# Kernel optimization log

Measured on AMD Instinct MI355X. Metric: run time of the kernel, lower is better.

The kernel has to match this reference:

```python
import jax, jax.numpy as jnp
import numpy as np

ALPHA = 32.0
LN_EPS = 1e-5

def _cdist(a, b):
    # a: [C, M, K], b: [C, N, K] -> [C, M, N] euclidean distances
    d2 = (jnp.sum(a * a, -1)[:, :, None]
          + jnp.sum(b * b, -1)[:, None, :]
          - 2.0 * jnp.einsum('cmk,cnk->cmn', a, b))
    return jnp.sqrt(jnp.maximum(d2, 1e-12))

def setup_inputs() -> dict:
    key = jax.random.key(0)
    k1, k2 = jax.random.split(key)
    B, D, H, W, C = 8, 16, 28, 28, 256
    CN, SS = 128, 28 * 28
    x = jax.random.normal(k1, (B, D, H, W, C), dtype=jnp.float32)
    ln_weight = jnp.ones((C,), dtype=jnp.float32)
    ln_bias = jnp.zeros((C,), dtype=jnp.float32)
    cluster_center = jax.random.uniform(k2, (C, CN, SS), dtype=jnp.float32)
    return {"x": x, "ln_weight": ln_weight, "ln_bias": ln_bias,
            "cluster_center": cluster_center}

def reference(x, ln_weight, ln_bias, cluster_center):
    B, D, H, W, C = x.shape
    CN = cluster_center.shape[1]
    # LayerNorm over last dim (feature_dim)
    mu = jnp.mean(x, -1, keepdims=True)
    var = jnp.mean(jnp.square(x - mu), -1, keepdims=True)
    xn = (x - mu) * jax.lax.rsqrt(var + LN_EPS) * ln_weight + ln_bias
    # B D H W C -> C (B D) (H W)
    x_re = jnp.transpose(xn, (4, 0, 1, 2, 3)).reshape(C, B * D, H * W)
    soft_assign = _cdist(x_re, cluster_center)          # [C, B*D, CN]
    # C (B D) CN -> B D C CN
    x_distance = jnp.transpose(soft_assign.reshape(C, B, D, CN), (1, 2, 0, 3))
    # NegSoftAssign: exp(-alpha*(x - min)) normalized == softmax(-alpha*x)
    x_distance_assign = jax.nn.softmax(-ALPHA * x_distance, axis=-1)
    cluster_dist = _cdist(cluster_center, cluster_center)  # [C, CN, CN]
    return (x_distance, x_distance_assign, cluster_dist)
```

## Files before the change

kernel.cpp:

```cpp
#include <hip/hip_runtime.h>
#include <hip/hip_bf16.h>
#include <math.h>

#define C_DIM 256
#define BD    128
#define HW    784
#define CN    128
#define KPAD  800

typedef short bf16x8 __attribute__((ext_vector_type(8)));
typedef float f32x4 __attribute__((ext_vector_type(4)));

__device__ inline ushort f2b(float f) {
  unsigned u = __float_as_uint(f);
  unsigned r = (u + 0x7FFFu + ((u >> 16) & 1u)) >> 16;
  return (ushort)r;
}

__global__ __launch_bounds__(256) void ln_transpose_kernel(
    const float* __restrict__ x, const float* __restrict__ lnw,
    const float* __restrict__ lnb, ushort* __restrict__ xre,
    float* __restrict__ anorm) {
  __shared__ ushort btile[256 * 66];
  __shared__ float nbuf[4][256];
  const int t = threadIdx.x, bd = blockIdx.y, bx = blockIdx.x;
  const int hw0 = bx * 64;
  const int w = t >> 6, lane = t & 63;
  const int q = lane >> 4, l = lane & 15;
  const bool last = (bx == 12);
  const int ngroups = last ? 1 : 4;
  const int rpw = ngroups * 4;
  float4 wv[4], bv[4];
  for (int s = 0; s < 4; ++s) {
    wv[s] = *(const float4*)(lnw + s * 64 + l * 4);
    bv[s] = *(const float4*)(lnb + s * 64 + l * 4);
  }
  float nrm[4][4];
  for (int s = 0; s < 4; ++s)
    for (int j = 0; j < 4; ++j) nrm[s][j] = 0.f;
  const float* xb = x + ((size_t)bd * HW + hw0) * 256 + l * 4;
  for (int g = 0; g < ngroups; ++g) {
    int r = w * rpw + g * 4 + q;
    float4 v[4];
    for (int s = 0; s < 4; ++s)
      v[s] = *(const float4*)(xb + (size_t)r * 256 + s * 64);
    float sum = 0.f;
    for (int s = 0; s < 4; ++s) sum += v[s].x + v[s].y + v[s].z + v[s].w;
    for (int off = 1; off <= 8; off <<= 1) sum += __shfl_xor(sum, off, 64);
    float mu = sum * (1.f / 256.f);
    float var = 0.f;
    for (int s = 0; s < 4; ++s) {
      float dx = v[s].x - mu, dy = v[s].y - mu, dz = v[s].z - mu, dw2 = v[s].w - mu;
      var += dx * dx + dy * dy + dz * dz + dw2 * dw2;
    }
    for (int off = 1; off <= 8; off <<= 1) var += __shfl_xor(var, off, 64);
    float sc = rsqrtf(var * (1.f / 256.f) + 1e-5f);
    for (int s = 0; s < 4; ++s) {
      float y0 = (v[s].x - mu) * sc * wv[s].x + bv[s].x;
      float y1 = (v[s].y - mu) * sc * wv[s].y + bv[s].y;
      float y2 = (v[s].z - mu) * sc * wv[s].z + bv[s].z;
      float y3 = (v[s].w - mu) * sc * wv[s].w + bv[s].w;
      nrm[s][0] = fmaf(y0, y0, nrm[s][0]);
      nrm[s][1] = fmaf(y1, y1, nrm[s][1]);
      nrm[s][2] = fmaf(y2, y2, nrm[s][2]);
      nrm[s][3] = fmaf(y3, y3, nrm[s][3]);
      int c = s * 64 + l * 4;
      btile[(c + 0) * 66 + r] = f2b(y0);
      btile[(c + 1) * 66 + r] = f2b(y1);
      btile[(c + 2) * 66 + r] = f2b(y2);
      btile[(c + 3) * 66 + r] = f2b(y3);
    }
  }
  for (int s = 0; s < 4; ++s)
    for (int j = 0; j < 4; ++j) {
      float v = nrm[s][j];
      v += __shfl_xor(v, 16, 64);
      v += __shfl_xor(v, 32, 64);
      nrm[s][j] = v;
    }
  if (q == 0)
    for (int s = 0; s < 4; ++s)
      for (int j = 0; j < 4; ++j) nbuf[w][s * 64 + l * 4 + j] = nrm[s][j];
  __syncthreads();
  float tot = nbuf[0][t] + nbuf[1][t] + nbuf[2][t] + nbuf[3][t];
  atomicAdd(&anorm[t * 128 + bd], tot);
  if (!last) {
    for (int i = 0; i < 32; ++i) {
      int c = w * 64 + i * 2 + (lane >> 5);
      int hwp = (lane & 31) * 2;
      uint val = *(const uint*)&btile[c * 66 + hwp];
      *(uint*)(xre + (size_t)c * (BD * KPAD) + (size_t)bd * KPAD + hw0 + hwp) = val;
    }
  } else {
    for (int i = 0; i < 8; ++i) {
      int c = w * 64 + i * 8 + (lane >> 3);
      int hwp = (lane & 7) * 2;
      uint val = *(const uint*)&btile[c * 66 + hwp];
      ushort* gp = xre + (size_t)c * (BD * KPAD) + (size_t)bd * KPAD + 768;
      *(uint*)(gp + hwp) = val;
      *(uint*)(gp + 16 + hwp) = 0u;
    }
  }
}

__global__ __launch_bounds__(256) void cc_convert_kernel(
    const float* __restrict__ cc, ushort* __restrict__ ccb,
    float* __restrict__ bnorm) {
  int b = blockIdx.x, c = b >> 2;
  int t = threadIdx.x, w = t >> 6, lane = t & 63;
  int r0 = (b & 3) * 32 + w * 8;
  for (int it = 0; it < 8; ++it) {
    int r = r0 + it;
    const float4* src = (const float4*)(cc + ((size_t)c * CN + r) * HW);
    ushort* dst = ccb + (size_t)c * (CN * KPAD) + (size_t)r * KPAD;
    float nrm = 0.f;
    for (int f = lane; f < 196; f += 64) {
      float4 v = src[f];
      nrm = fmaf(v.x, v.x, nrm); nrm = fmaf(v.y, v.y, nrm);
      nrm = fmaf(v.z, v.z, nrm); nrm = fmaf(v.w, v.w, nrm);
      ushort4 o; o.x = f2b(v.x); o.y = f2b(v.y); o.z = f2b(v.z); o.w = f2b(v.w);
      *(ushort4*)(dst + f * 4) = o;
    }
    for (int off = 32; off >= 1; off >>= 1) nrm += __shfl_xor(nrm, off, 64);
    if (lane == 0) bnorm[c * 128 + r] = nrm;
    if (lane < 4) *(ushort4*)(dst + 784 + lane * 4) = make_ushort4(0, 0, 0, 0);
  }
}

__global__ __launch_bounds__(256, 2) void gemm_mfma_kernel(
    const ushort* __restrict__ xre, const ushort* __restrict__ ccb,
    const float* __restrict__ anorm, const float* __restrict__ bnorm,
    float* __restrict__ out_d, float* __restrict__ out_s,
    float* __restrict__ out_c) {
  __shared__ __align__(16) ushort At[512 * 8];
  __shared__ __align__(16) ushort Bt[512 * 8];
  __shared__ float smin[2][128];
  __shared__ float ssum[2][128];
  const int c = blockIdx.x, mode = blockIdx.y;
  const int t = threadIdx.x, w = t >> 6, lane = t & 63;
  const int quad = lane >> 4, ln = lane & 15;
  const int wrow = (w >> 1) * 64, wcol = (w & 1) * 64;
  const ushort* Ag = (mode ? ccb : xre) + (size_t)c * (128 * KPAD);
  const ushort* Bg = ccb + (size_t)c * (128 * KPAD);

  f32x4 acc[4][4];
  for (int i = 0; i < 4; ++i)
    for (int j = 0; j < 4; ++j) acc[i][j] = f32x4{0.f, 0.f, 0.f, 0.f};

  const int ci0 = 128 * w;
  const int row0 = (ci0 + lane) >> 2;
  const int row1 = (ci0 + 64 + lane) >> 2;
  const int q0 = (lane & 3) ^ (row0 & 3);
  const int q1 = (lane & 3) ^ (row1 & 3);
  const ushort* ga0 = Ag + (size_t)row0 * KPAD + q0 * 8;
  const ushort* ga1 = Ag + (size_t)row1 * KPAD + q1 * 8;
  const ushort* gb0 = Bg + (size_t)row0 * KPAD + q0 * 8;
  const ushort* gb1 = Bg + (size_t)row1 * KPAD + q1 * 8;
  ushort* la0 = &At[ci0 * 8];
  ushort* la1 = &At[(ci0 + 64) * 8];
  ushort* lb0 = &Bt[ci0 * 8];
  ushort* lb1 = &Bt[(ci0 + 64) * 8];

  for (int k0 = 0; k0 < 25; ++k0) {
    __syncthreads();
    int kb = k0 * 32;
    __builtin_amdgcn_global_load_lds(
        (const __attribute__((address_space(1))) unsigned int*)(ga0 + kb),
        (__attribute__((address_space(3))) unsigned int*)la0, 16, 0, 0);
    __builtin_amdgcn_global_load_lds(
        (const __attribute__((address_space(1))) unsigned int*)(ga1 + kb),
        (__attribute__((address_space(3))) unsigned int*)la1, 16, 0, 0);
    __builtin_amdgcn_global_load_lds(
        (const __attribute__((address_space(1))) unsigned int*)(gb0 + kb),
        (__attribute__((address_space(3))) unsigned int*)lb0, 16, 0, 0);
    __builtin_amdgcn_global_load_lds(
        (const __attribute__((address_space(1))) unsigned int*)(gb1 + kb),
        (__attribute__((address_space(3))) unsigned int*)lb1, 16, 0, 0);
    __syncthreads();
    bf16x8 af[4], bf[4];
    for (int i = 0; i < 4; ++i) {
      int m = wrow + i * 16 + ln;
      af[i] = *(const bf16x8*)&At[(m * 4 + (quad ^ (m & 3))) * 8];
    }
    for (int j = 0; j < 4; ++j) {
      int n = wcol + j * 16 + ln;
      bf[j] = *(const bf16x8*)&Bt[(n * 4 + (quad ^ (n & 3))) * 8];
    }
    for (int i = 0; i < 4; ++i)
      for (int j = 0; j < 4; ++j)
        acc[i][j] = __builtin_amdgcn_mfma_f32_16x16x32_bf16(af[i], bf[j], acc[i][j], 0, 0, 0);
  }

  const float* rn = (mode ? bnorm : anorm) + c * 128;
  const float* cn = bnorm + c * 128;
  float cnv[4];
  for (int j = 0; j < 4; ++j) cnv[j] = cn[wcol + j * 16 + ln];
  float d[4][4][4];
  for (int i = 0; i < 4; ++i) {
    float rv[4];
    for (int r = 0; r < 4; ++r) rv[r] = rn[wrow + i * 16 + quad * 4 + r];
    for (int j = 0; j < 4; ++j)
      for (int r = 0; r < 4; ++r) {
        float d2 = rv[r] + cnv[j] - 2.f * acc[i][j][r];
        d[i][j][r] = sqrtf(fmaxf(d2, 1e-12f));
      }
  }

  if (mode) {
    float* ob = out_c + (size_t)c * (128 * 128);
    for (int i = 0; i < 4; ++i)
      for (int r = 0; r < 4; ++r) {
        int m = wrow + i * 16 + quad * 4 + r;
        for (int j = 0; j < 4; ++j) ob[m * 128 + wcol + j * 16 + ln] = d[i][j][r];
      }
  } else {
    int half = w & 1;
    for (int i = 0; i < 4; ++i)
      for (int r = 0; r < 4; ++r) {
        int m = wrow + i * 16 + quad * 4 + r;
        size_t ob = ((size_t)m * 256 + c) * 128 + wcol;
        for (int j = 0; j < 4; ++j) out_d[ob + j * 16 + ln] = d[i][j][r];
        float mn = fminf(fminf(d[i][0][r], d[i][1][r]), fminf(d[i][2][r], d[i][3][r]));
        for (int off = 1; off < 16; off <<= 1) mn = fminf(mn, __shfl_xor(mn, off, 64));
        if (ln == 0) smin[half][m] = mn;
      }
    __syncthreads();
    for (int i = 0; i < 4; ++i)
      for (int r = 0; r < 4; ++r) {
        int m = wrow + i * 16 + quad * 4 + r;
        float mn = fminf(smin[0][m], smin[1][m]);
        float s = 0.f;
        for (int j = 0; j < 4; ++j) {
          float e = __expf(-32.f * (d[i][j][r] - mn));
          d[i][j][r] = e;
          s += e;
        }
        for (int off = 1; off < 16; off <<= 1) s += __shfl_xor(s, off, 64);
        if (ln == 0) ssum[half][m] = s;
      }
    __syncthreads();
    for (int i = 0; i < 4; ++i)
      for (int r = 0; r < 4; ++r) {
        int m = wrow + i * 16 + quad * 4 + r;
        float inv = 1.f / (ssum[0][m] + ssum[1][m]);
        size_t ob = ((size_t)m * 256 + c) * 128 + wcol;
        for (int j = 0; j < 4; ++j) out_s[ob + j * 16 + ln] = d[i][j][r] * inv;
      }
  }
}

extern "C" void kernel_launch(void* const* d_in, const int* in_sizes, int n_in,
                              void* d_out, int out_size, void* d_ws, size_t ws_size,
                              hipStream_t stream) {
  const float* x   = (const float*)d_in[0];
  const float* lnw = (const float*)d_in[1];
  const float* lnb = (const float*)d_in[2];
  const float* cc  = (const float*)d_in[3];
  float* out   = (float*)d_out;
  float* out_d = out;
  float* out_s = out + 4194304;
  float* out_c = out + 8388608;

  ushort* xre_b = (ushort*)d_ws;
  ushort* cc_b  = xre_b + 26214400;
  float*  anorm = (float*)(cc_b + 26214400);
  float*  bnorm = anorm + 32768;

  hipMemsetAsync(anorm, 0, 32768 * sizeof(float), stream);
  ln_transpose_kernel<<<dim3(13, 128), 256, 0, stream>>>(x, lnw, lnb, xre_b, anorm);
  cc_convert_kernel<<<1024, 256, 0, stream>>>(cc, cc_b, bnorm);
  gemm_mfma_kernel<<<dim3(256, 2), 256, 0, stream>>>(xre_b, cc_b, anorm, bnorm,
                                                     out_d, out_s, out_c);
}
```

Before: 309.9 us.

## Double-buffer GEMM LDS loads, shrink LN/convert tiles, single-pass LN stats

The GEMM now double-buffers its LDS tiles, prefetching the next K slice while the current one feeds the MFMAs, and drops one barrier per iteration. Mode-1 blocks (cluster vs cluster) skip loading B and reuse the A tile. The grid is flattened so each cluster's two modes are adjacent, which may share the center tile in cache. The LayerNorm/transpose kernel uses 32-wide HW tiles with more blocks and computes variance in one pass as E[x^2]-mu^2, which is slightly less numerically robust. The cc conversion is spread over twice as many blocks, one row per 16 lanes.

```diff
diff --git a/kernel.cpp b/kernel.cpp
--- a/kernel.cpp
+++ b/kernel.cpp
@@ -21,15 +21,18 @@
     const float* __restrict__ x, const float* __restrict__ lnw,
     const float* __restrict__ lnb, ushort* __restrict__ xre,
     float* __restrict__ anorm) {
-  __shared__ ushort btile[256 * 66];
+  __shared__ ushort btile[256 * 36];
   __shared__ float nbuf[4][256];
   const int t = threadIdx.x, bd = blockIdx.y, bx = blockIdx.x;
-  const int hw0 = bx * 64;
+  const int hw0 = bx * 32;
   const int w = t >> 6, lane = t & 63;
   const int q = lane >> 4, l = lane & 15;
-  const bool last = (bx == 12);
-  const int ngroups = last ? 1 : 4;
+  const bool last = (bx == 24);
+  const int ngroups = last ? 1 : 2;
   const int rpw = ngroups * 4;
+  if (last) {
+    for (int r = 16; r < 32; ++r) btile[t * 36 + r] = 0;
+  }
   float4 wv[4], bv[4];
   for (int s = 0; s < 4; ++s) {
     wv[s] = *(const float4*)(lnw + s * 64 + l * 4);
@@ -44,17 +47,19 @@
     float4 v[4];
     for (int s = 0; s < 4; ++s)
       v[s] = *(const float4*)(xb + (size_t)r * 256 + s * 64);
-    float sum = 0.f;
-    for (int s = 0; s < 4; ++s) sum += v[s].x + v[s].y + v[s].z + v[s].w;
-    for (int off = 1; off <= 8; off <<= 1) sum += __shfl_xor(sum, off, 64);
+    float sum = 0.f, sq = 0.f;
+    for (int s = 0; s < 4; ++s) {
+      sum += v[s].x + v[s].y + v[s].z + v[s].w;
+      sq = fmaf(v[s].x, v[s].x, sq); sq = fmaf(v[s].y, v[s].y, sq);
+      sq = fmaf(v[s].z, v[s].z, sq); sq = fmaf(v[s].w, v[s].w, sq);
+    }
+    for (int off = 1; off <= 8; off <<= 1) {
+      sum += __shfl_xor(sum, off, 64);
+      sq  += __shfl_xor(sq, off, 64);
+    }
     float mu = sum * (1.f / 256.f);
-    float var = 0.f;
-    for (int s = 0; s < 4; ++s) {
-      float dx = v[s].x - mu, dy = v[s].y - mu, dz = v[s].z - mu, dw2 = v[s].w - mu;
-      var += dx * dx + dy * dy + dz * dz + dw2 * dw2;
-    }
-    for (int off = 1; off <= 8; off <<= 1) var += __shfl_xor(var, off, 64);
-    float sc = rsqrtf(var * (1.f / 256.f) + 1e-5f);
+    float var = fmaf(-mu, mu, sq * (1.f / 256.f));
+    float sc = rsqrtf(var + 1e-5f);
     for (int s = 0; s < 4; ++s) {
       float y0 = (v[s].x - mu) * sc * wv[s].x + bv[s].x;
       float y1 = (v[s].y - mu) * sc * wv[s].y + bv[s].y;
@@ -65,10 +70,10 @@
       nrm[s][2] = fmaf(y2, y2, nrm[s][2]);
       nrm[s][3] = fmaf(y3, y3, nrm[s][3]);
       int c = s * 64 + l * 4;
-      btile[(c + 0) * 66 + r] = f2b(y0);
-      btile[(c + 1) * 66 + r] = f2b(y1);
-      btile[(c + 2) * 66 + r] = f2b(y2);
-      btile[(c + 3) * 66 + r] = f2b(y3);
+      btile[(c + 0) * 36 + r] = f2b(y0);
+      btile[(c + 1) * 36 + r] = f2b(y1);
+      btile[(c + 2) * 36 + r] = f2b(y2);
+      btile[(c + 3) * 36 + r] = f2b(y3);
     }
   }
   for (int s = 0; s < 4; ++s)
@@ -84,47 +89,37 @@
   __syncthreads();
   float tot = nbuf[0][t] + nbuf[1][t] + nbuf[2][t] + nbuf[3][t];
   atomicAdd(&anorm[t * 128 + bd], tot);
-  if (!last) {
-    for (int i = 0; i < 32; ++i) {
-      int c = w * 64 + i * 2 + (lane >> 5);
-      int hwp = (lane & 31) * 2;
-      uint val = *(const uint*)&btile[c * 66 + hwp];
-      *(uint*)(xre + (size_t)c * (BD * KPAD) + (size_t)bd * KPAD + hw0 + hwp) = val;
-    }
-  } else {
-    for (int i = 0; i < 8; ++i) {
-      int c = w * 64 + i * 8 + (lane >> 3);
-      int hwp = (lane & 7) * 2;
-      uint val = *(const uint*)&btile[c * 66 + hwp];
-      ushort* gp = xre + (size_t)c * (BD * KPAD) + (size_t)bd * KPAD + 768;
-      *(uint*)(gp + hwp) = val;
-      *(uint*)(gp + 16 + hwp) = 0u;
-    }
+  for (int i = 0; i < 8; ++i) {
+    int c = w * 64 + i * 8 + (lane >> 3);
+    int ho = (lane & 7) * 4;
+    ushort4 val = *(const ushort4*)&btile[c * 36 + ho];
+    *(ushort4*)(xre + (size_t)c * (BD * KPAD) + (size_t)bd * KPAD + hw0 + ho) = val;
   }
 }
 
 __global__ __launch_bounds__(256) void cc_convert_kernel(
     const float* __restrict__ cc, ushort* __restrict__ ccb,
     float* __restrict__ bnorm) {
-  int b = blockIdx.x, c = b >> 2;
+  int b = blockIdx.x, c = b >> 3;
   int t = threadIdx.x, w = t >> 6, lane = t & 63;
-  int r0 = (b & 3) * 32 + w * 8;
-  for (int it = 0; it < 8; ++it) {
-    int r = r0 + it;
-    const float4* src = (const float4*)(cc + ((size_t)c * CN + r) * HW);
-    ushort* dst = ccb + (size_t)c * (CN * KPAD) + (size_t)r * KPAD;
-    float nrm = 0.f;
-    for (int f = lane; f < 196; f += 64) {
+  int q = lane >> 4, l = lane & 15;
+  int r = (b & 7) * 16 + w * 4 + q;
+  const float4* src = (const float4*)(cc + ((size_t)c * CN + r) * HW);
+  ushort* dst = ccb + ((size_t)c * CN + r) * KPAD;
+  float nrm = 0.f;
+  for (int i = 0; i < 13; ++i) {
+    int f = i * 16 + l;
+    if (f < 196) {
       float4 v = src[f];
       nrm = fmaf(v.x, v.x, nrm); nrm = fmaf(v.y, v.y, nrm);
       nrm = fmaf(v.z, v.z, nrm); nrm = fmaf(v.w, v.w, nrm);
       ushort4 o; o.x = f2b(v.x); o.y = f2b(v.y); o.z = f2b(v.z); o.w = f2b(v.w);
       *(ushort4*)(dst + f * 4) = o;
     }
-    for (int off = 32; off >= 1; off >>= 1) nrm += __shfl_xor(nrm, off, 64);
-    if (lane == 0) bnorm[c * 128 + r] = nrm;
-    if (lane < 4) *(ushort4*)(dst + 784 + lane * 4) = make_ushort4(0, 0, 0, 0);
-  }
+  }
+  for (int off = 1; off <= 8; off <<= 1) nrm += __shfl_xor(nrm, off, 64);
+  if (l == 0) bnorm[c * 128 + r] = nrm;
+  if (l < 4) *(ushort4*)(dst + 784 + l * 4) = make_ushort4(0, 0, 0, 0);
 }
 
 __global__ __launch_bounds__(256, 2) void gemm_mfma_kernel(
@@ -132,11 +127,12 @@
     const float* __restrict__ anorm, const float* __restrict__ bnorm,
     float* __restrict__ out_d, float* __restrict__ out_s,
     float* __restrict__ out_c) {
-  __shared__ __align__(16) ushort At[512 * 8];
-  __shared__ __align__(16) ushort Bt[512 * 8];
+  __shared__ __align__(16) ushort At[2][4096];
+  __shared__ __align__(16) ushort Bt[2][4096];
   __shared__ float smin[2][128];
   __shared__ float ssum[2][128];
-  const int c = blockIdx.x, mode = blockIdx.y;
+  const int bx = blockIdx.x;
+  const int c = bx >> 1, mode = bx & 1;
   const int t = threadIdx.x, w = t >> 6, lane = t & 63;
   const int quad = lane >> 4, ln = lane & 15;
   const int wrow = (w >> 1) * 64, wcol = (w & 1) * 64;
@@ -156,40 +152,47 @@
   const ushort* ga1 = Ag + (size_t)row1 * KPAD + q1 * 8;
   const ushort* gb0 = Bg + (size_t)row0 * KPAD + q0 * 8;
   const ushort* gb1 = Bg + (size_t)row1 * KPAD + q1 * 8;
-  ushort* la0 = &At[ci0 * 8];
-  ushort* la1 = &At[(ci0 + 64) * 8];
-  ushort* lb0 = &Bt[ci0 * 8];
-  ushort* lb1 = &Bt[(ci0 + 64) * 8];
-
+  const int la0 = ci0 * 8, la1 = (ci0 + 64) * 8;
+
+#define ISSUE(k, p)                                                          \
+  do {                                                                       \
+    int kb = (k) * 32;                                                       \
+    __builtin_amdgcn_global_load_lds(                                        \
+        (const __attribute__((address_space(1))) unsigned int*)(ga0 + kb),   \
+        (__attribute__((address_space(3))) unsigned int*)&At[p][la0], 16, 0, 0); \
+    __builtin_amdgcn_global_load_lds(                                        \
+        (const __attribute__((address_space(1))) unsigned int*)(ga1 + kb),   \
+        (__attribute__((address_space(3))) unsigned int*)&At[p][la1], 16, 0, 0); \
+    if (!mode) {                                                             \
+      __builtin_amdgcn_global_load_lds(                                      \
+          (const __attribute__((address_space(1))) unsigned int*)(gb0 + kb), \
+          (__attribute__((address_space(3))) unsigned int*)&Bt[p][la0], 16, 0, 0); \
+      __builtin_amdgcn_global_load_lds(                                      \
+          (const __attribute__((address_space(1))) unsigned int*)(gb1 + kb), \
+          (__attribute__((address_space(3))) unsigned int*)&Bt[p][la1], 16, 0, 0); \
+    }                                                                        \
+  } while (0)
+
+  ISSUE(0, 0);
   for (int k0 = 0; k0 < 25; ++k0) {
     __syncthreads();
-    int kb = k0 * 32;
-    __builtin_amdgcn_global_load_lds(
-        (const __attribute__((address_space(1))) unsigned int*)(ga0 + kb),
-        (__attribute__((address_space(3))) unsigned int*)la0, 16, 0, 0);
-    __builtin_amdgcn_global_load_lds(
-        (const __attribute__((address_space(1))) unsigned int*)(ga1 + kb),
-        (__attribute__((address_space(3))) unsigned int*)la1, 16, 0, 0);
-    __builtin_amdgcn_global_load_lds(
-        (const __attribute__((address_space(1))) unsigned int*)(gb0 + kb),
-        (__attribute__((address_space(3))) unsigned int*)lb0, 16, 0, 0);
-    __builtin_amdgcn_global_load_lds(
-        (const __attribute__((address_space(1))) unsigned int*)(gb1 + kb),
-        (__attribute__((address_space(3))) unsigned int*)lb1, 16, 0, 0);
-    __syncthreads();
+    if (k0 < 24) ISSUE(k0 + 1, (k0 + 1) & 1);
+    const ushort* Ab = At[k0 & 1];
+    const ushort* Bb = mode ? At[k0 & 1] : Bt[k0 & 1];
     bf16x8 af[4], bf[4];
     for (int i = 0; i < 4; ++i) {
       int m = wrow + i * 16 + ln;
-      af[i] = *(const bf16x8*)&At[(m * 4 + (quad ^ (m & 3))) * 8];
+      af[i] = *(const bf16x8*)&Ab[(m * 4 + (quad ^ (m & 3))) * 8];
     }
     for (int j = 0; j < 4; ++j) {
       int n = wcol + j * 16 + ln;
-      bf[j] = *(const bf16x8*)&Bt[(n * 4 + (quad ^ (n & 3))) * 8];
+      bf[j] = *(const bf16x8*)&Bb[(n * 4 + (quad ^ (n & 3))) * 8];
     }
     for (int i = 0; i < 4; ++i)
       for (int j = 0; j < 4; ++j)
         acc[i][j] = __builtin_amdgcn_mfma_f32_16x16x32_bf16(af[i], bf[j], acc[i][j], 0, 0, 0);
   }
+#undef ISSUE
 
   const float* rn = (mode ? bnorm : anorm) + c * 128;
   const float* cn = bnorm + c * 128;
@@ -267,8 +270,8 @@
   float*  bnorm = anorm + 32768;
 
   hipMemsetAsync(anorm, 0, 32768 * sizeof(float), stream);
-  ln_transpose_kernel<<<dim3(13, 128), 256, 0, stream>>>(x, lnw, lnb, xre_b, anorm);
-  cc_convert_kernel<<<1024, 256, 0, stream>>>(cc, cc_b, bnorm);
-  gemm_mfma_kernel<<<dim3(256, 2), 256, 0, stream>>>(xre_b, cc_b, anorm, bnorm,
-                                                     out_d, out_s, out_c);
-}
+  ln_transpose_kernel<<<dim3(25, 128), 256, 0, stream>>>(x, lnw, lnb, xre_b, anorm);
+  cc_convert_kernel<<<2048, 256, 0, stream>>>(cc, cc_b, bnorm);
+  gemm_mfma_kernel<<<512, 256, 0, stream>>>(xre_b, cc_b, anorm, bnorm,
+                                            out_d, out_s, out_c);
+}
```

New measurement: 320.0 us. 1.03x slower.
